# Kernel tuning notes

Measured on AMD Instinct MI355X. Metric: run time of the kernel, lower is better.

## Reference

```python
import jax, jax.numpy as jnp
import numpy as np

B, C, H, W = 16, 512, 32, 32
EPS = 1e-5

def setup_inputs() -> dict:
    key = jax.random.key(0)
    ks = jax.random.split(key, 7)
    s = 1.0 / np.sqrt(C)
    return {
        "x": jax.random.normal(ks[0], (B, C, H, W), dtype=jnp.float32),
        "norm_w": jnp.ones((C,), jnp.float32),
        "norm_b": jnp.zeros((C,), jnp.float32),
        "qkv_w": jax.random.normal(ks[1], (3 * C, C), dtype=jnp.float32) * s,
        "qkv_b": jax.random.normal(ks[2], (3 * C,), dtype=jnp.float32) * 0.01,
        "out_w": jax.random.normal(ks[3], (C, C), dtype=jnp.float32) * s,
        "out_b": jax.random.normal(ks[4], (C,), dtype=jnp.float32) * 0.01,
    }

def reference(x, norm_w, norm_b, qkv_w, qkv_b, out_w, out_b):
    b, c, h, w = x.shape
    # GroupNorm with num_groups=1: normalize over (C,H,W) per sample, per-channel affine
    mean = jnp.mean(x, axis=(1, 2, 3), keepdims=True)
    var = jnp.var(x, axis=(1, 2, 3), keepdims=True)
    xn = (x - mean) * jax.lax.rsqrt(var + EPS)
    xn = xn * norm_w[None, :, None, None] + norm_b[None, :, None, None]
    # 1x1 conv QKV: [b,3c,h,w]
    qkv = jnp.einsum('bchw,oc->bohw', xn, qkv_w) + qkv_b[None, :, None, None]
    q, k, v = jnp.split(qkv, 3, axis=1)
    n = h * w
    q = q.transpose(0, 2, 3, 1).reshape(b, n, c)   # [b, N, c]
    k = k.reshape(b, c, n)                          # [b, c, N]
    v = v.transpose(0, 2, 3, 1).reshape(b, n, c)   # [b, N, c]
    scores = jnp.einsum('bnc,bcm->bnm', q, k) * (c ** -0.5)  # [b, N, N]
    attn = jax.nn.softmax(scores, axis=-1)
    out = jnp.einsum('bnm,bmc->bnc', attn, v)       # [b, N, c]
    out = out.reshape(b, h, w, c).transpose(0, 3, 1, 2)
    out = jnp.einsum('bchw,oc->bohw', out, out_w) + out_b[None, :, None, None]
    return out + x
```

## Files before the change

kernel.cpp:

```cpp
#include <hip/hip_runtime.h>
#include <math.h>

#define BATCH 16
#define CH    512
#define NTOK  1024
#define CHW   (CH * NTOK)
#define EPSV  1e-5f

typedef __attribute__((ext_vector_type(8))) short bf16x8;
typedef __attribute__((ext_vector_type(4))) float f32x4;

__device__ __forceinline__ unsigned short f2bf(float f) {
    union { float f; unsigned u; } cv; cv.f = f;
    unsigned r = cv.u + 0x7FFFu + ((cv.u >> 16) & 1u);
    return (unsigned short)(r >> 16);
}

__device__ __forceinline__ void async16(const unsigned short* g, unsigned short* l) {
    __builtin_amdgcn_global_load_lds(
        (const __attribute__((address_space(1))) void*)g,
        (__attribute__((address_space(3))) void*)l,
        16, 0, 0);
}


static const size_t OFF_WQKV = 256;
static const size_t OFF_OW   = OFF_WQKV + 1572864;
static const size_t OFF_XNT  = OFF_OW   + 524288;
static const size_t OFF_QT   = OFF_XNT  + 16777216;
static const size_t OFF_KT   = OFF_QT   + 16777216;
static const size_t OFF_V    = OFF_KT   + 16777216;
static const size_t OFF_OT   = OFF_V    + 16777216;

__global__ __launch_bounds__(256) void k_stats_partial(const float* __restrict__ x, float* __restrict__ ws) {
    int blk   = blockIdx.x;
    int b     = blk >> 6;
    int chunk = blk & 63;
    const float4* xp = (const float4*)(x + (size_t)b * CHW + (size_t)chunk * 8192);
    int t = threadIdx.x;
    float s = 0.0f, ss = 0.0f;
#pragma unroll
    for (int j = 0; j < 8; j++) {
        float4 v = xp[t + j * 256];
        s  += v.x + v.y + v.z + v.w;
        ss += v.x * v.x + v.y * v.y + v.z * v.z + v.w * v.w;
    }
#pragma unroll
    for (int off = 32; off; off >>= 1) {
        s  += __shfl_xor(s, off, 64);
        ss += __shfl_xor(ss, off, 64);
    }
    __shared__ float ls[4], lss[4];
    int wave = t >> 6, lane = t & 63;
    if (lane == 0) { ls[wave] = s; lss[wave] = ss; }
    __syncthreads();
    if (t == 0) {
        atomicAdd(&ws[b], ls[0] + ls[1] + ls[2] + ls[3]);
        atomicAdd(&ws[16 + b], lss[0] + lss[1] + lss[2] + lss[3]);
    }
}

__global__ __launch_bounds__(256) void k_cvt2(const float* __restrict__ wq, const float* __restrict__ wo,
                                              unsigned short* __restrict__ WQ, unsigned short* __restrict__ WO,
                                              float* __restrict__ stats) {
    if (blockIdx.x == 0 && threadIdx.x < 64) stats[threadIdx.x] = 0.0f;
    int i = blockIdx.x * 256 + threadIdx.x;
    const float* src; unsigned short* dst; int off;
    if (i < 196608) { src = wq; dst = WQ; off = i; }
    else            { src = wo; dst = WO; off = i - 196608; }
    float4 v = ((const float4*)src)[off];
    ushort4 o;
    o.x = f2bf(v.x); o.y = f2bf(v.y); o.z = f2bf(v.z); o.w = f2bf(v.w);
    ((ushort4*)dst)[off] = o;
}

__global__ __launch_bounds__(256) void k_xnt(const float* __restrict__ x,
                                             const float* __restrict__ nw,
                                             const float* __restrict__ nb,
                                             const float* __restrict__ ws,
                                             unsigned short* __restrict__ xnt) {
    __shared__ float ls[64][65];
    int b  = blockIdx.z;
    int c0 = blockIdx.y * 64;
    int n0 = blockIdx.x * 64;
    const float inv = 1.0f / (float)CHW;
    float mean = ws[b] * inv;
    float rstd = rsqrtf(ws[16 + b] * inv - mean * mean + EPSV);
    int t = threadIdx.x;
    int cl = t >> 4, n4 = t & 15;
    const float* xb = x + (size_t)b * CHW;
#pragma unroll
    for (int i = 0; i < 4; i++) {
        int c = c0 + cl + i * 16;
        float a  = rstd * nw[c];
        float bb = nb[c] - mean * a;
        float4 v = *(const float4*)(xb + (size_t)c * NTOK + n0 + n4 * 4);
        ls[cl + i * 16][n4 * 4 + 0] = v.x * a + bb;
        ls[cl + i * 16][n4 * 4 + 1] = v.y * a + bb;
        ls[cl + i * 16][n4 * 4 + 2] = v.z * a + bb;
        ls[cl + i * 16][n4 * 4 + 3] = v.w * a + bb;
    }
    __syncthreads();
    int nl = t >> 4, c4 = t & 15;
    unsigned short* dst = xnt + (size_t)b * NTOK * CH;
#pragma unroll
    for (int i = 0; i < 4; i++) {
        int n = n0 + nl + i * 16;
        ushort4 o;
        o.x = f2bf(ls[c4 * 4 + 0][nl + i * 16]);
        o.y = f2bf(ls[c4 * 4 + 1][nl + i * 16]);
        o.z = f2bf(ls[c4 * 4 + 2][nl + i * 16]);
        o.w = f2bf(ls[c4 * 4 + 3][nl + i * 16]);
        *(ushort4*)(dst + (size_t)n * CH + c0 + c4 * 4) = o;
    }
}

__device__ __forceinline__ void mfma_core2(const unsigned short* __restrict__ A, int lda,
                                           const unsigned short* __restrict__ B, int ldb,
                                           int K, int m0, int n0,
                                           unsigned short* sm,
                                           f32x4 acc[4][8]) {
    const int t = threadIdx.x;
    const int w = t >> 6, lane = t & 63;
    const int wm = (w & 1) * 64, wn = (w >> 1) * 128;
    const int r16 = lane & 15, quad = lane >> 4;
#pragma unroll
    for (int i = 0; i < 4; i++)
#pragma unroll
        for (int j = 0; j < 8; j++) acc[i][j] = (f32x4){0.f, 0.f, 0.f, 0.f};
    const int sr = lane >> 2;
    const int sk = (((lane & 3) ^ ((lane >> 3) & 3))) * 8;
    const int swz = ((quad ^ (r16 >> 1)) & 3) * 8;
    const unsigned short* gA0 = A + (size_t)(m0 + w * 32 + sr) * lda + sk;
    const unsigned short* gA1 = gA0 + (size_t)16 * lda;
    const unsigned short* gB0 = B + (size_t)(n0 + w * 64 + sr) * ldb + sk;
    const unsigned short* gB1 = gB0 + (size_t)16 * ldb;
    const unsigned short* gB2 = gB0 + (size_t)32 * ldb;
    const unsigned short* gB3 = gB0 + (size_t)48 * ldb;
    unsigned short* lA0 = sm + (w * 32) * 32;
    unsigned short* lA1 = sm + (w * 32 + 16) * 32;
    unsigned short* lB0 = sm + 8192 + (w * 64) * 32;
    unsigned short* lB1 = lB0 + 16 * 32;
    unsigned short* lB2 = lB0 + 32 * 32;
    unsigned short* lB3 = lB0 + 48 * 32;
    const int T = K >> 5;
    async16(gA0, lA0); async16(gA1, lA1);
    async16(gB0, lB0); async16(gB1, lB1); async16(gB2, lB2); async16(gB3, lB3);
    for (int tt = 0; tt < T; tt++) {
        __syncthreads();
        const int ab = (tt & 1) << 12;
        const int bb = (tt & 1) << 13;
        if (tt + 1 < T) {
            const int nab = ab ^ 4096, nbb = bb ^ 8192;
            const int ko = (tt + 1) << 5;
            async16(gA0 + ko, lA0 + nab); async16(gA1 + ko, lA1 + nab);
            async16(gB0 + ko, lB0 + nbb); async16(gB1 + ko, lB1 + nbb);
            async16(gB2 + ko, lB2 + nbb); async16(gB3 + ko, lB3 + nbb);
        }
        bf16x8 af[4], bfr[8];
#pragma unroll
        for (int i = 0; i < 4; i++) af[i]  = *(const bf16x8*)(sm + ab + (wm + i * 16 + r16) * 32 + swz);
#pragma unroll
        for (int j = 0; j < 8; j++) bfr[j] = *(const bf16x8*)(sm + 8192 + bb + (wn + j * 16 + r16) * 32 + swz);
#pragma unroll
        for (int i = 0; i < 4; i++)
#pragma unroll
            for (int j = 0; j < 8; j++)
                acc[i][j] = __builtin_amdgcn_mfma_f32_16x16x32_bf16(af[i], bfr[j], acc[i][j], 0, 0, 0);
    }
}

#define TS1 136
#define TS2 264

__global__ __launch_bounds__(256, 2) void k_gemm_qkv(const unsigned short* __restrict__ Wq,
                                                     const float* __restrict__ qb,
                                                     const unsigned short* __restrict__ XNT,
                                                     unsigned short* __restrict__ QT,
                                                     unsigned short* __restrict__ KT,
                                                     unsigned short* __restrict__ V) {
    __shared__ __align__(16) unsigned short smem[256 * TS1];
    const int b  = blockIdx.z;
    const int m0 = blockIdx.y * 128;
    const int n0 = blockIdx.x * 256;
    f32x4 acc[4][8];
    mfma_core2(Wq, CH, XNT + (size_t)b * NTOK * CH, CH, CH, m0, n0, smem, acc);
    const int t = threadIdx.x;
    const int w = t >> 6, lane = t & 63;
    const int wm = (w & 1) * 64, wn = (w >> 1) * 128;
    const int r16 = lane & 15, quad = lane >> 4;
    const int region = m0 >> 9;
    __syncthreads();
    if (region < 2) {
#pragma unroll
        for (int i = 0; i < 4; i++) {
            const int ol = wm + i * 16 + quad * 4;
            const int og = m0 + ol;
            const float b0 = qb[og], b1 = qb[og + 1], b2 = qb[og + 2], b3 = qb[og + 3];
#pragma unroll
            for (int j = 0; j < 8; j++) {
                const int nl = wn + j * 16 + r16;
                f32x4 a = acc[i][j];
                ushort4 pk;
                pk.x = f2bf(a[0] + b0); pk.y = f2bf(a[1] + b1);
                pk.z = f2bf(a[2] + b2); pk.w = f2bf(a[3] + b3);
                *(ushort4*)(smem + nl * TS1 + ol) = pk;
            }
        }
        __syncthreads();
        unsigned short* dst = ((region == 0) ? QT : KT) + (size_t)b * NTOK * CH + (size_t)n0 * CH + (m0 & 511);
#pragma unroll
        for (int p = 0; p < 32; p++) {
            const int row = (t >> 5) + p * 8;
            const int seg = (t & 31) * 4;
            *(ushort4*)(dst + (size_t)row * CH + seg) = *(const ushort4*)(smem + row * TS1 + seg);
        }
    } else {
#pragma unroll
        for (int i = 0; i < 4; i++) {
            const int ol = wm + i * 16 + quad * 4;
            const int og = m0 + ol;
#pragma unroll
            for (int j = 0; j < 8; j++) {
                const int nl = wn + j * 16 + r16;
                f32x4 a = acc[i][j];
#pragma unroll
                for (int r = 0; r < 4; r++)
                    smem[(ol + r) * TS2 + nl] = f2bf(a[r] + qb[og + r]);
            }
        }
        __syncthreads();
        unsigned short* dst = V + (size_t)b * CH * NTOK + (size_t)(m0 & 511) * NTOK + n0;
#pragma unroll
        for (int p = 0; p < 32; p++) {
            const int row = (t >> 5) + (p & 15) * 8;
            const int seg = (t & 31) * 4 + (p >> 4) * 128;
            *(ushort4*)(dst + (size_t)row * NTOK + seg) = *(const ushort4*)(smem + row * TS2 + seg);
        }
    }
}

__global__ __launch_bounds__(512, 1) void k_attn(const unsigned short* __restrict__ QT,
                                                 const unsigned short* __restrict__ KTg,
                                                 const unsigned short* __restrict__ Vg,
                                                 unsigned short* __restrict__ OT) {
    __shared__ __align__(16) unsigned short sm[70400];
    unsigned short* smK = sm;
    unsigned short* smV = sm + 32768;
    unsigned short* smP = sm + 65536;
    float* lsum2 = (float*)(sm + 69888);

    const int bid = blockIdx.x;
    const int xcd = bid & 7, slot = bid >> 3;
    const int b   = xcd * 2 + (slot & 1);
    const int q0  = (slot >> 1) * 64;

    const int t = threadIdx.x;
    const int w = t >> 6, lane = t & 63;
    const int qg = w & 1, h = w >> 1;
    const int r16 = lane & 15, quad = lane >> 4;
    const int srow = lane >> 2;
    const int sc   = (((lane & 3) ^ ((lane >> 3) & 3))) * 8;
    const int swz  = ((quad ^ (r16 >> 1)) & 3) * 8;

    const unsigned short* Qb = QT  + (size_t)b * NTOK * CH;
    const unsigned short* Kb = KTg + (size_t)b * NTOK * CH;
    const unsigned short* Vb = Vg  + (size_t)b * CH * NTOK;

    bf16x8 qf[2][16];
    {
        const unsigned short* qrow0 = Qb + (size_t)(q0 + qg * 32 + r16) * CH + quad * 8;
        const unsigned short* qrow1 = qrow0 + (size_t)16 * CH;
#pragma unroll
        for (int kc = 0; kc < 16; kc++) {
            qf[0][kc] = *(const bf16x8*)(qrow0 + kc * 32);
            qf[1][kc] = *(const bf16x8*)(qrow1 + kc * 32);
        }
    }

    f32x4 accO[16];
#pragma unroll
    for (int j = 0; j < 16; j++) accO[j] = (f32x4){0.f, 0.f, 0.f, 0.f};
    float lsum[2][4] = {{0.f, 0.f, 0.f, 0.f}, {0.f, 0.f, 0.f, 0.f}};
    const float scale = 0.044194173824159216f;

#pragma unroll
    for (int i = 0; i < 8; i++) {
        const int ch = w * 8 + i, g = ch >> 4, kc = ch & 15;
        async16(Kb + (size_t)(g * 16 + srow) * CH + kc * 32 + sc, smK + ch * 512);
    }
    __syncthreads();

    for (int kt = 0; kt < 16; kt++) {
        {
            const unsigned short* vbase = Vb + (size_t)kt * 64;
#pragma unroll
            for (int cgi = 0; cgi < 4; cgi++) {
                const int cg = w * 4 + cgi;
#pragma unroll
                for (int kk = 0; kk < 2; kk++)
                    async16(vbase + (size_t)(cg * 16 + srow) * NTOK + kk * 32 + sc,
                            smV + (cg * 2 + kk) * 512);
            }
        }
        f32x4 accS[2];
        accS[0] = (f32x4){0.f, 0.f, 0.f, 0.f};
        accS[1] = (f32x4){0.f, 0.f, 0.f, 0.f};
#pragma unroll
        for (int kc = 0; kc < 16; kc++) {
            bf16x8 kf = *(const bf16x8*)(smK + (h * 16 + kc) * 512 + r16 * 32 + swz);
            accS[0] = __builtin_amdgcn_mfma_f32_16x16x32_bf16(qf[0][kc], kf, accS[0], 0, 0, 0);
            accS[1] = __builtin_amdgcn_mfma_f32_16x16x32_bf16(qf[1][kc], kf, accS[1], 0, 0, 0);
        }
#pragma unroll
        for (int qs = 0; qs < 2; qs++) {
#pragma unroll
            for (int r = 0; r < 4; r++) {
                float e = __expf(accS[qs][r] * scale);
                lsum[qs][r] += e;
                smP[(qg * 32 + qs * 16 + quad * 4 + r) * 68 + h * 16 + r16] = f2bf(e);
            }
        }
        __syncthreads();
        if (kt < 15) {
            const unsigned short* kbase = Kb + (size_t)(kt + 1) * 64 * CH;
#pragma unroll
            for (int i = 0; i < 8; i++) {
                const int ch = w * 8 + i, g = ch >> 4, kc = ch & 15;
                async16(kbase + (size_t)(g * 16 + srow) * CH + kc * 32 + sc, smK + ch * 512);
            }
        }
        bf16x8 pf[4][2];
#pragma unroll
        for (int qj = 0; qj < 4; qj++)
#pragma unroll
            for (int kk = 0; kk < 2; kk++)
                pf[qj][kk] = *(const bf16x8*)(smP + (qj * 16 + r16) * 68 + kk * 32 + quad * 8);
#pragma unroll
        for (int cj = 0; cj < 4; cj++) {
            bf16x8 vf0 = *(const bf16x8*)(smV + ((w * 4 + cj) * 2 + 0) * 512 + r16 * 32 + swz);
            bf16x8 vf1 = *(const bf16x8*)(smV + ((w * 4 + cj) * 2 + 1) * 512 + r16 * 32 + swz);
#pragma unroll
            for (int qj = 0; qj < 4; qj++) {
                accO[qj * 4 + cj] = __builtin_amdgcn_mfma_f32_16x16x32_bf16(pf[qj][0], vf0, accO[qj * 4 + cj], 0, 0, 0);
                accO[qj * 4 + cj] = __builtin_amdgcn_mfma_f32_16x16x32_bf16(pf[qj][1], vf1, accO[qj * 4 + cj], 0, 0, 0);
            }
        }
        __syncthreads();
    }

#pragma unroll
    for (int qs = 0; qs < 2; qs++)
#pragma unroll
        for (int r = 0; r < 4; r++) {
            float v = lsum[qs][r];
            v += __shfl_xor(v, 1, 64);
            v += __shfl_xor(v, 2, 64);
            v += __shfl_xor(v, 4, 64);
            v += __shfl_xor(v, 8, 64);
            if (r16 == 0) lsum2[h * 64 + qg * 32 + qs * 16 + quad * 4 + r] = v;
        }
    __syncthreads();
#pragma unroll
    for (int qj = 0; qj < 4; qj++) {
        float iv[4];
#pragma unroll
        for (int r = 0; r < 4; r++) {
            const int row = qj * 16 + quad * 4 + r;
            iv[r] = 1.0f / (lsum2[row] + lsum2[64 + row] + lsum2[128 + row] + lsum2[192 + row]);
        }
#pragma unroll
        for (int cj = 0; cj < 4; cj++) {
            f32x4 a = accO[qj * 4 + cj];
#pragma unroll
            for (int r = 0; r < 4; r++)
                sm[(qj * 16 + quad * 4 + r) * 520 + w * 64 + cj * 16 + r16] = f2bf(a[r] * iv[r]);
        }
    }
    __syncthreads();
    unsigned short* dst = OT + (size_t)b * NTOK * CH + (size_t)q0 * CH;
#pragma unroll
    for (int p = 0; p < 16; p++) {
        const int row = (t >> 7) + p * 4;
        const int seg = (t & 127) * 4;
        *(ushort4*)(dst + (size_t)row * CH + seg) = *(const ushort4*)(sm + row * 520 + seg);
    }
}

__global__ __launch_bounds__(256, 2) void k_gemm_out(const unsigned short* __restrict__ OW,
                                                     const float* __restrict__ ob,
                                                     const unsigned short* __restrict__ OT,
                                                     const float* __restrict__ x,
                                                     float* __restrict__ out) {
    __shared__ __align__(16) unsigned short smem[24576];
    const int b  = blockIdx.z;
    const int m0 = blockIdx.y * 128;
    const int n0 = blockIdx.x * 256;
    f32x4 acc[4][8];
    mfma_core2(OW, CH, OT + (size_t)b * NTOK * CH, CH, CH, m0, n0, smem, acc);
    const int t = threadIdx.x;
    const int w = t >> 6, lane = t & 63;
    const int wm = (w & 1) * 64, wn = (w >> 1) * 128;
    const int r16 = lane & 15, quad = lane >> 4;
#pragma unroll
    for (int i = 0; i < 4; i++) {
        const int o0g = m0 + wm + i * 16 + quad * 4;
#pragma unroll
        for (int j = 0; j < 8; j++) {
            const int col = n0 + wn + j * 16 + r16;
            f32x4 a = acc[i][j];
#pragma unroll
            for (int r = 0; r < 4; r++) {
                size_t idx = (size_t)b * CHW + (size_t)(o0g + r) * NTOK + col;
                out[idx] = a[r] + ob[o0g + r] + x[idx];
            }
        }
    }
}

extern "C" void kernel_launch(void* const* d_in, const int* in_sizes, int n_in,
                              void* d_out, int out_size, void* d_ws, size_t ws_size,
                              hipStream_t stream) {
    const float* x      = (const float*)d_in[0];
    const float* norm_w = (const float*)d_in[1];
    const float* norm_b = (const float*)d_in[2];
    const float* qkv_w  = (const float*)d_in[3];
    const float* qkv_b  = (const float*)d_in[4];
    const float* out_w  = (const float*)d_in[5];
    const float* out_b  = (const float*)d_in[6];
    float* out = (float*)d_out;
    char* wsb  = (char*)d_ws;

    float* stats = (float*)wsb;
    unsigned short* WQ  = (unsigned short*)(wsb + OFF_WQKV);
    unsigned short* OW  = (unsigned short*)(wsb + OFF_OW);
    unsigned short* XNT = (unsigned short*)(wsb + OFF_XNT);
    unsigned short* QT  = (unsigned short*)(wsb + OFF_QT);
    unsigned short* KT  = (unsigned short*)(wsb + OFF_KT);
    unsigned short* V   = (unsigned short*)(wsb + OFF_V);
    unsigned short* OT  = (unsigned short*)(wsb + OFF_OT);

    k_cvt2<<<1024, 256, 0, stream>>>(qkv_w, out_w, WQ, OW, stats);
    k_stats_partial<<<BATCH * 64, 256, 0, stream>>>(x, stats);
    k_xnt<<<dim3(NTOK / 64, CH / 64, BATCH), 256, 0, stream>>>(x, norm_w, norm_b, stats, XNT);
    k_gemm_qkv<<<dim3(NTOK / 256, 3 * CH / 128, BATCH), 256, 0, stream>>>(WQ, qkv_b, XNT, QT, KT, V);
    k_attn<<<256, 512, 0, stream>>>(QT, KT, V, OT);
    k_gemm_out<<<dim3(NTOK / 256, CH / 128, BATCH), 256, 0, stream>>>(OW, out_b, OT, x, out);
}
```

Baseline: 249.2 us.

## Halve attention block tile to 32 queries, 256 threads, two blocks per CU

The attention kernel is retiled. Each block now handles 32 queries with 4 waves, and 512 blocks are launched with two resident per CU, instead of 64 queries with 8 waves and one block per CU. Key/value tiles shrink from 64 to 32 keys, so there are 32 loop iterations, and the shared memory footprint is roughly halved. The aim is to let two independent blocks overlap their barriers and loads, at the cost of twice the K/V reload traffic per query and more synchronisations per key.

```diff
diff --git a/kernel.cpp b/kernel.cpp
--- a/kernel.cpp
+++ b/kernel.cpp
@@ -240,24 +240,25 @@
     }
 }
 
-__global__ __launch_bounds__(512, 1) void k_attn(const unsigned short* __restrict__ QT,
+#define PS 40
+__global__ __launch_bounds__(256, 2) void k_attn(const unsigned short* __restrict__ QT,
                                                  const unsigned short* __restrict__ KTg,
                                                  const unsigned short* __restrict__ Vg,
                                                  unsigned short* __restrict__ OT) {
-    __shared__ __align__(16) unsigned short sm[70400];
+    __shared__ __align__(16) unsigned short sm[34176];
     unsigned short* smK = sm;
-    unsigned short* smV = sm + 32768;
-    unsigned short* smP = sm + 65536;
-    float* lsum2 = (float*)(sm + 69888);
+    unsigned short* smV = sm + 16384;
+    unsigned short* smP = sm + 32768;
+    float* lsum2 = (float*)(sm + 34048);
 
     const int bid = blockIdx.x;
     const int xcd = bid & 7, slot = bid >> 3;
     const int b   = xcd * 2 + (slot & 1);
-    const int q0  = (slot >> 1) * 64;
+    const int q0  = (slot >> 1) * 32;
 
     const int t = threadIdx.x;
     const int w = t >> 6, lane = t & 63;
-    const int qg = w & 1, h = w >> 1;
+    const int qg = w & 1, kg = w >> 1;
     const int r16 = lane & 15, quad = lane >> 4;
     const int srow = lane >> 2;
     const int sc   = (((lane & 3) ^ ((lane >> 3) & 3))) * 8;
@@ -267,21 +268,18 @@
     const unsigned short* Kb = KTg + (size_t)b * NTOK * CH;
     const unsigned short* Vb = Vg  + (size_t)b * CH * NTOK;
 
-    bf16x8 qf[2][16];
+    bf16x8 qf[16];
     {
-        const unsigned short* qrow0 = Qb + (size_t)(q0 + qg * 32 + r16) * CH + quad * 8;
-        const unsigned short* qrow1 = qrow0 + (size_t)16 * CH;
-#pragma unroll
-        for (int kc = 0; kc < 16; kc++) {
-            qf[0][kc] = *(const bf16x8*)(qrow0 + kc * 32);
-            qf[1][kc] = *(const bf16x8*)(qrow1 + kc * 32);
-        }
+        const unsigned short* qrow = Qb + (size_t)(q0 + qg * 16 + r16) * CH + quad * 8;
+#pragma unroll
+        for (int kc = 0; kc < 16; kc++)
+            qf[kc] = *(const bf16x8*)(qrow + kc * 32);
     }
 
     f32x4 accO[16];
 #pragma unroll
     for (int j = 0; j < 16; j++) accO[j] = (f32x4){0.f, 0.f, 0.f, 0.f};
-    float lsum[2][4] = {{0.f, 0.f, 0.f, 0.f}, {0.f, 0.f, 0.f, 0.f}};
+    float lsum[4] = {0.f, 0.f, 0.f, 0.f};
     const float scale = 0.044194173824159216f;
 
 #pragma unroll
@@ -291,97 +289,78 @@
     }
     __syncthreads();
 
-    for (int kt = 0; kt < 16; kt++) {
+    for (int kt = 0; kt < 32; kt++) {
         {
-            const unsigned short* vbase = Vb + (size_t)kt * 64;
-#pragma unroll
-            for (int cgi = 0; cgi < 4; cgi++) {
-                const int cg = w * 4 + cgi;
-#pragma unroll
-                for (int kk = 0; kk < 2; kk++)
-                    async16(vbase + (size_t)(cg * 16 + srow) * NTOK + kk * 32 + sc,
-                            smV + (cg * 2 + kk) * 512);
+            const unsigned short* vbase = Vb + (size_t)kt * 32;
+#pragma unroll
+            for (int i = 0; i < 8; i++) {
+                const int cg = w * 8 + i;
+                async16(vbase + (size_t)(cg * 16 + srow) * NTOK + sc, smV + cg * 512);
             }
         }
-        f32x4 accS[2];
-        accS[0] = (f32x4){0.f, 0.f, 0.f, 0.f};
-        accS[1] = (f32x4){0.f, 0.f, 0.f, 0.f};
+        f32x4 accS = (f32x4){0.f, 0.f, 0.f, 0.f};
 #pragma unroll
         for (int kc = 0; kc < 16; kc++) {
-            bf16x8 kf = *(const bf16x8*)(smK + (h * 16 + kc) * 512 + r16 * 32 + swz);
-            accS[0] = __builtin_amdgcn_mfma_f32_16x16x32_bf16(qf[0][kc], kf, accS[0], 0, 0, 0);
-            accS[1] = __builtin_amdgcn_mfma_f32_16x16x32_bf16(qf[1][kc], kf, accS[1], 0, 0, 0);
-        }
-#pragma unroll
-        for (int qs = 0; qs < 2; qs++) {
-#pragma unroll
-            for (int r = 0; r < 4; r++) {
-                float e = __expf(accS[qs][r] * scale);
-                lsum[qs][r] += e;
-                smP[(qg * 32 + qs * 16 + quad * 4 + r) * 68 + h * 16 + r16] = f2bf(e);
-            }
+            bf16x8 kf = *(const bf16x8*)(smK + (kg * 16 + kc) * 512 + r16 * 32 + swz);
+            accS = __builtin_amdgcn_mfma_f32_16x16x32_bf16(qf[kc], kf, accS, 0, 0, 0);
+        }
+#pragma unroll
+        for (int r = 0; r < 4; r++) {
+            float e = __expf(accS[r] * scale);
+            lsum[r] += e;
+            smP[(qg * 16 + quad * 4 + r) * PS + kg * 16 + r16] = f2bf(e);
         }
         __syncthreads();
-        if (kt < 15) {
-            const unsigned short* kbase = Kb + (size_t)(kt + 1) * 64 * CH;
+        if (kt < 31) {
+            const unsigned short* kbase = Kb + (size_t)(kt + 1) * 32 * CH;
 #pragma unroll
             for (int i = 0; i < 8; i++) {
                 const int ch = w * 8 + i, g = ch >> 4, kc = ch & 15;
                 async16(kbase + (size_t)(g * 16 + srow) * CH + kc * 32 + sc, smK + ch * 512);
             }
         }
-        bf16x8 pf[4][2];
-#pragma unroll
-        for (int qj = 0; qj < 4; qj++)
-#pragma unroll
-            for (int kk = 0; kk < 2; kk++)
-                pf[qj][kk] = *(const bf16x8*)(smP + (qj * 16 + r16) * 68 + kk * 32 + quad * 8);
-#pragma unroll
-        for (int cj = 0; cj < 4; cj++) {
-            bf16x8 vf0 = *(const bf16x8*)(smV + ((w * 4 + cj) * 2 + 0) * 512 + r16 * 32 + swz);
-            bf16x8 vf1 = *(const bf16x8*)(smV + ((w * 4 + cj) * 2 + 1) * 512 + r16 * 32 + swz);
-#pragma unroll
-            for (int qj = 0; qj < 4; qj++) {
-                accO[qj * 4 + cj] = __builtin_amdgcn_mfma_f32_16x16x32_bf16(pf[qj][0], vf0, accO[qj * 4 + cj], 0, 0, 0);
-                accO[qj * 4 + cj] = __builtin_amdgcn_mfma_f32_16x16x32_bf16(pf[qj][1], vf1, accO[qj * 4 + cj], 0, 0, 0);
-            }
+        bf16x8 pf0 = *(const bf16x8*)(smP + (r16)      * PS + quad * 8);
+        bf16x8 pf1 = *(const bf16x8*)(smP + (16 + r16) * PS + quad * 8);
+#pragma unroll
+        for (int cj = 0; cj < 8; cj++) {
+            bf16x8 vf = *(const bf16x8*)(smV + (w * 8 + cj) * 512 + r16 * 32 + swz);
+            accO[cj]     = __builtin_amdgcn_mfma_f32_16x16x32_bf16(pf0, vf, accO[cj], 0, 0, 0);
+            accO[8 + cj] = __builtin_amdgcn_mfma_f32_16x16x32_bf16(pf1, vf, accO[8 + cj], 0, 0, 0);
         }
         __syncthreads();
     }
 
 #pragma unroll
-    for (int qs = 0; qs < 2; qs++)
-#pragma unroll
-        for (int r = 0; r < 4; r++) {
-            float v = lsum[qs][r];
-            v += __shfl_xor(v, 1, 64);
-            v += __shfl_xor(v, 2, 64);
-            v += __shfl_xor(v, 4, 64);
-            v += __shfl_xor(v, 8, 64);
-            if (r16 == 0) lsum2[h * 64 + qg * 32 + qs * 16 + quad * 4 + r] = v;
-        }
-    __syncthreads();
-#pragma unroll
-    for (int qj = 0; qj < 4; qj++) {
+    for (int r = 0; r < 4; r++) {
+        float v = lsum[r];
+        v += __shfl_xor(v, 1, 64);
+        v += __shfl_xor(v, 2, 64);
+        v += __shfl_xor(v, 4, 64);
+        v += __shfl_xor(v, 8, 64);
+        if (r16 == 0) lsum2[kg * 32 + qg * 16 + quad * 4 + r] = v;
+    }
+    __syncthreads();
+#pragma unroll
+    for (int qj = 0; qj < 2; qj++) {
         float iv[4];
 #pragma unroll
         for (int r = 0; r < 4; r++) {
             const int row = qj * 16 + quad * 4 + r;
-            iv[r] = 1.0f / (lsum2[row] + lsum2[64 + row] + lsum2[128 + row] + lsum2[192 + row]);
-        }
-#pragma unroll
-        for (int cj = 0; cj < 4; cj++) {
-            f32x4 a = accO[qj * 4 + cj];
+            iv[r] = 1.0f / (lsum2[row] + lsum2[32 + row]);
+        }
+#pragma unroll
+        for (int cj = 0; cj < 8; cj++) {
+            f32x4 a = accO[qj * 8 + cj];
 #pragma unroll
             for (int r = 0; r < 4; r++)
-                sm[(qj * 16 + quad * 4 + r) * 520 + w * 64 + cj * 16 + r16] = f2bf(a[r] * iv[r]);
+                sm[(qj * 16 + quad * 4 + r) * 520 + w * 128 + cj * 16 + r16] = f2bf(a[r] * iv[r]);
         }
     }
     __syncthreads();
     unsigned short* dst = OT + (size_t)b * NTOK * CH + (size_t)q0 * CH;
 #pragma unroll
     for (int p = 0; p < 16; p++) {
-        const int row = (t >> 7) + p * 4;
+        const int row = (t >> 7) + p * 2;
         const int seg = (t & 127) * 4;
         *(ushort4*)(dst + (size_t)row * CH + seg) = *(const ushort4*)(sm + row * 520 + seg);
     }
@@ -444,6 +423,6 @@
     k_stats_partial<<<BATCH * 64, 256, 0, stream>>>(x, stats);
     k_xnt<<<dim3(NTOK / 64, CH / 64, BATCH), 256, 0, stream>>>(x, norm_w, norm_b, stats, XNT);
     k_gemm_qkv<<<dim3(NTOK / 256, 3 * CH / 128, BATCH), 256, 0, stream>>>(WQ, qkv_b, XNT, QT, KT, V);
-    k_attn<<<256, 512, 0, stream>>>(QT, KT, V, OT);
+    k_attn<<<512, 256, 0, stream>>>(QT, KT, V, OT);
     k_gemm_out<<<dim3(NTOK / 256, CH / 128, BATCH), 256, 0, stream>>>(OW, out_b, OT, x, out);
 }
```

Result: faster. 228.3 us (-8.4%).
